# Optimization experiments

Measured on AMD Instinct MI355X. Metric: run time of the kernel, lower is better.

The kernel has to match this reference:

```python
import jax, jax.numpy as jnp
import numpy as np

B, S, E, H = 1, 2048, 4096, 32
D = E // H
MAX_POS = 2048
NEG_MASK = -66504.0
SCALE = float(np.sqrt(D))


def _rope(x, position_ids):
    # x: [B, S, H, D]; GPT-NeoX style rotate-half rotary embedding
    half = D // 2
    inv_freq = 1.0 / (10000.0 ** (jnp.arange(0, half, dtype=jnp.float32) * 2.0 / D))  # [D/2]
    ang = position_ids.astype(jnp.float32)[:, None] * inv_freq[None, :]               # [S, D/2]
    cos = jnp.cos(ang)[None, :, None, :]
    sin = jnp.sin(ang)[None, :, None, :]
    x1, x2 = x[..., :half], x[..., half:]
    return jnp.concatenate([x1 * cos - x2 * sin, x2 * cos + x1 * sin], axis=-1)


def setup_inputs() -> dict:
    key = jax.random.key(0)
    ks = jax.random.split(key, 9)
    s = 0.02
    return {
        "hidden_states": jax.random.normal(ks[0], (B, S, E), jnp.float32),
        "wq": jax.random.normal(ks[1], (E, E), jnp.float32) * s,
        "bq": jnp.zeros((E,), jnp.float32),
        "wk": jax.random.normal(ks[2], (E, E), jnp.float32) * s,
        "bk": jnp.zeros((E,), jnp.float32),
        "wv": jax.random.normal(ks[3], (E, E), jnp.float32) * s,
        "bv": jnp.zeros((E,), jnp.float32),
        "wo": jax.random.normal(ks[4], (E, E), jnp.float32) * s,
        "bo": jnp.zeros((E,), jnp.float32),
        "position_ids": jnp.arange(S, dtype=jnp.int32),
    }


def reference(hidden_states, wq, bq, wk, bk, wv, bv, wo, bo, position_ids):
    # QKV projections (nn.Linear: x @ W.T + b)
    q = hidden_states @ wq.T + bq
    k = hidden_states @ wk.T + bk
    v = hidden_states @ wv.T + bv
    # [B, S, H, D]
    q = q.reshape(B, S, H, D)
    k = k.reshape(B, S, H, D)
    v = v.reshape(B, S, H, D)
    # rotary embedding on key and query
    q = _rope(q, position_ids)
    k = _rope(k, position_ids)
    # [B, H, S, D]
    q = q.transpose(0, 2, 1, 3)
    k = k.transpose(0, 2, 1, 3)
    v = v.transpose(0, 2, 1, 3)
    # attention scores; causal mask added BEFORE dividing by scale (faithful to source)
    scores = jnp.einsum("bhqd,bhkd->bhqk", q, k)
    causal = (1.0 - jnp.tril(jnp.ones((S, S), jnp.float32))) * NEG_MASK  # [S, S]
    scores = (scores + causal[None, None]) / SCALE
    attn = jax.nn.softmax(scores.astype(jnp.float32), axis=-1).astype(q.dtype)
    ctx = jnp.einsum("bhqk,bhkd->bhqd", attn, v)
    ctx = ctx.transpose(0, 2, 1, 3).reshape(B, S, E)
    return ctx @ wo.T + bo
```

## Files before the change

### kernel.cpp

```cpp
#include <hip/hip_runtime.h>
#include <hip/hip_bf16.h>

constexpr int SEQ = 2048;
constexpr int EMB = 4096;
constexpr int NH  = 32;
constexpr int HD  = 128;
constexpr int HALF = 64;

typedef __bf16 bf16x8 __attribute__((ext_vector_type(8)));
typedef float  f32x4  __attribute__((ext_vector_type(4)));
using u16 = unsigned short;
typedef u16 ushort8 __attribute__((ext_vector_type(8)));
typedef u16 u16x4 __attribute__((ext_vector_type(4)));

__device__ inline float bf2f(u16 u) {
  union { unsigned int i; float f; } v; v.i = ((unsigned int)u) << 16; return v.f;
}
__device__ inline u16 f2bf(float f) {
  union { __bf16 b; u16 u; } v; v.b = (__bf16)f; return v.u;
}

#define GLL16(gp, lp) __builtin_amdgcn_global_load_lds( \
    (const __attribute__((address_space(1))) void*)(gp), \
    (__attribute__((address_space(3))) void*)(lp), 16, 0, 0)

__global__ void k_f32_to_bf16(const float* __restrict__ in, u16* __restrict__ out, int n) {
  int i = (blockIdx.x * blockDim.x + threadIdx.x) * 8;
  if (i >= n) return;
  f32x4 a = *(const f32x4*)(in + i);
  f32x4 b = *(const f32x4*)(in + i + 4);
  ushort8 o;
  o[0] = f2bf(a[0]); o[1] = f2bf(a[1]); o[2] = f2bf(a[2]); o[3] = f2bf(a[3]);
  o[4] = f2bf(b[0]); o[5] = f2bf(b[1]); o[6] = f2bf(b[2]); o[7] = f2bf(b[3]);
  *(ushort8*)(out + i) = o;
}

__global__ void k_rope_table(const int* __restrict__ pos, float* __restrict__ tab) {
  int idx = blockIdx.x * blockDim.x + threadIdx.x;
  if (idx >= SEQ * HALF) return;
  int s = idx >> 6, d = idx & 63;
  double invf = pow(10000.0, -(double)d / 64.0);
  double ang = (double)pos[s] * invf;
  tab[idx * 2]     = (float)cos(ang);
  tab[idx * 2 + 1] = (float)sin(ang);
}

__global__ void k_rope(u16* __restrict__ X, const float* __restrict__ tab, float scale) {
  int idx = blockIdx.x * blockDim.x + threadIdx.x;
  if (idx >= SEQ * NH * HALF) return;
  int d = idx & 63;
  int h = (idx >> 6) & 31;
  int s = idx >> 11;
  u16* p = X + (size_t)s * EMB + h * HD + d;
  float x1 = bf2f(p[0]), x2 = bf2f(p[HALF]);
  float c  = tab[(s * HALF + d) * 2];
  float sn = tab[(s * HALF + d) * 2 + 1];
  p[0]    = f2bf((x1 * c - x2 * sn) * scale);
  p[HALF] = f2bf((x2 * c + x1 * sn) * scale);
}

template<int TBM, int TBN>
__global__ __launch_bounds__(256) void k_gemm(
    const u16* __restrict__ A, const u16* __restrict__ W,
    const float* __restrict__ b0, const float* __restrict__ b1, const float* __restrict__ b2,
    void* __restrict__ C0, void* __restrict__ C1, void* __restrict__ C2,
    int M, int N, int K, int mode)
{
  constexpr int CH_A = TBM / 16, CH_B = TBN / 16;
  constexpr int CH_W = (CH_A + CH_B) / 4;
  constexpr int MA = TBM / 32, NB = TBN / 32;
  __shared__ alignas(16) u16 As[TBM * 32];
  __shared__ alignas(16) u16 Bs[TBN * 32];
  int tid = threadIdx.x;
  int lane = tid & 63, wid = tid >> 6;
  int wm = wid >> 1, wn = wid & 1;
  int l15 = lane & 15, lhi = lane >> 4;

  int nwg = gridDim.x * gridDim.y;
  int lin = blockIdx.y * gridDim.x + blockIdx.x;
  int cpx = nwg >> 3;
  int swz = (lin & 7) * cpx + (lin >> 3);
  int bx = swz % gridDim.x, by = swz / gridDim.x;
  int m0 = by * TBM, n0 = bx * TBN;

  f32x4 acc[MA][NB] = {};

  int srow = lane >> 2;
  int scol = (lane & 3) * 8;

  for (int k0 = 0; k0 < K; k0 += 32) {
    __syncthreads();
#pragma unroll
    for (int i = 0; i < CH_W; i++) {
      int chunk = wid * CH_W + i;
      if (chunk < CH_A) {
        int row = chunk * 16 + srow;
        GLL16(A + (size_t)(m0 + row) * K + k0 + scol, As + chunk * 512);
      } else {
        int c2 = chunk - CH_A;
        int row = c2 * 16 + srow;
        GLL16(W + (size_t)(n0 + row) * K + k0 + scol, Bs + c2 * 512);
      }
    }
    __syncthreads();

    bf16x8 af[MA], bfr[NB];
#pragma unroll
    for (int a = 0; a < MA; a++)
      af[a] = *(const bf16x8*)&As[(wm * (TBM / 2) + a * 16 + l15) * 32 + lhi * 8];
#pragma unroll
    for (int b = 0; b < NB; b++)
      bfr[b] = *(const bf16x8*)&Bs[(wn * (TBN / 2) + b * 16 + l15) * 32 + lhi * 8];
#pragma unroll
    for (int a = 0; a < MA; a++)
#pragma unroll
      for (int b = 0; b < NB; b++)
        acc[a][b] = __builtin_amdgcn_mfma_f32_16x16x32_bf16(af[a], bfr[b], acc[a][b], 0, 0, 0);
  }

  const float* bias = b0;
  void* Cout = C0;
  int mode_l = mode, Nn = N, n_base = n0;
  if (mode == 3) {
    int seg = n0 >> 12;
    Nn = EMB; n_base = n0 & 4095;
    if (seg == 0)      { bias = b0; Cout = C0; mode_l = 0; }
    else if (seg == 1) { bias = b1; Cout = C1; mode_l = 0; }
    else               { bias = b2; Cout = C2; mode_l = 2; }
  }

#pragma unroll
  for (int a = 0; a < MA; a++) {
    int m = m0 + wm * (TBM / 2) + a * 16 + lhi * 4;
#pragma unroll
    for (int b = 0; b < NB; b++) {
      int n = n_base + wn * (TBN / 2) + b * 16 + l15;
      float bs = bias[n];
      if (mode_l == 2) {
        u16x4 pk;
#pragma unroll
        for (int r = 0; r < 4; r++) pk[r] = f2bf(acc[a][b][r] + bs);
        *(u16x4*)&((u16*)Cout)[(size_t)n * M + m] = pk;
      } else if (mode_l == 1) {
#pragma unroll
        for (int r = 0; r < 4; r++)
          ((float*)Cout)[(size_t)(m + r) * Nn + n] = acc[a][b][r] + bs;
      } else {
#pragma unroll
        for (int r = 0; r < 4; r++)
          ((u16*)Cout)[(size_t)(m + r) * Nn + n] = f2bf(acc[a][b][r] + bs);
      }
    }
  }
}

constexpr int QB = 64, KVB = 64;

__global__ __launch_bounds__(256) void k_flash(
    const u16* __restrict__ Q, const u16* __restrict__ K, const u16* __restrict__ VT,
    u16* __restrict__ ctx)
{
  __shared__ alignas(16) u16 Ks[2][KVB * 128];
  __shared__ alignas(16) u16 Vt[2][HD * 64];
  __shared__ alignas(16) u16 Pl[4][16 * 64];

  int tid = threadIdx.x, lane = tid & 63, wid = tid >> 6;
  int l15 = lane & 15, lhi = lane >> 4;
  int h = blockIdx.y;

  auto stage = [&](int buf, int t2) {
    int kv = t2 * KVB;
#pragma unroll
    for (int it = 0; it < 4; it++) {
      int chunk = tid + it * 256;
      int r = chunk >> 4, bp = chunk & 15;
      GLL16(K + (size_t)(kv + r) * EMB + h * HD + (((bp - r) & 15) << 3), &Ks[buf][chunk * 8]);
    }
#pragma unroll
    for (int it = 0; it < 4; it++) {
      int chunk = tid + it * 256;
      int d = chunk >> 3, bp = chunk & 7;
      GLL16(VT + (size_t)(h * HD + d) * SEQ + kv + (((bp - d) & 7) << 3), &Vt[buf][chunk * 8]);
    }
  };

  for (int pi = 0; pi < 2; pi++) {
    int qb = pi ? (int)blockIdx.x : 31 - (int)blockIdx.x;
    int q0 = qb * QB;
    int qw = q0 + wid * 16;

    bf16x8 qf[4];
#pragma unroll
    for (int kc = 0; kc < 4; kc++)
      qf[kc] = *(const bf16x8*)&Q[(size_t)(qw + l15) * EMB + h * HD + kc * 32 + lhi * 8];

    f32x4 O[8] = {};
    float mrow[4], lrow[4];
#pragma unroll
    for (int r = 0; r < 4; r++) { mrow[r] = -3.0e38f; lrow[r] = 0.f; }

    int nt = qb + 1;
    __syncthreads();
    stage(0, 0);
    for (int t = 0; t < nt; t++) {
      __syncthreads();
      if (t + 1 < nt) stage((t + 1) & 1, t + 1);

      const u16* ks = Ks[t & 1];
      const u16* vt = Vt[t & 1];
      float p[4][4];
      bool need_mask = (t == nt - 1);
#pragma unroll
      for (int c = 0; c < 4; c++) {
        f32x4 s = {};
        int r0 = c * 16 + l15;
#pragma unroll
        for (int kc = 0; kc < 4; kc++) {
          bf16x8 kf = *(const bf16x8*)&ks[r0 * 128 + (((kc * 4 + lhi) + r0) & 15) * 8];
          s = __builtin_amdgcn_mfma_f32_16x16x32_bf16(qf[kc], kf, s, 0, 0, 0);
        }
#pragma unroll
        for (int r = 0; r < 4; r++) {
          float sv = s[r];
          if (need_mask) {
            int qg = qw + lhi * 4 + r;
            int kg = t * KVB + c * 16 + l15;
            if (kg > qg) sv = -3.0e38f;
          }
          p[c][r] = sv;
        }
      }
      float fscale[4];
#pragma unroll
      for (int r = 0; r < 4; r++) {
        float m = fmaxf(fmaxf(p[0][r], p[1][r]), fmaxf(p[2][r], p[3][r]));
#pragma unroll
        for (int x = 1; x < 16; x <<= 1) m = fmaxf(m, __shfl_xor(m, x, 64));
        float mnew = fmaxf(mrow[r], m);
        fscale[r] = __expf(mrow[r] - mnew);
        mrow[r] = mnew;
      }
#pragma unroll
      for (int c = 0; c < 4; c++)
#pragma unroll
        for (int r = 0; r < 4; r++)
          p[c][r] = __expf(p[c][r] - mrow[r]);
#pragma unroll
      for (int r = 0; r < 4; r++) {
        float s = p[0][r] + p[1][r] + p[2][r] + p[3][r];
#pragma unroll
        for (int x = 1; x < 16; x <<= 1) s += __shfl_xor(s, x, 64);
        lrow[r] = lrow[r] * fscale[r] + s;
      }
#pragma unroll
      for (int d = 0; d < 8; d++)
#pragma unroll
        for (int r = 0; r < 4; r++)
          O[d][r] *= fscale[r];
#pragma unroll
      for (int c = 0; c < 4; c++) {
        int kb = c * 2 + (l15 >> 3), klo = l15 & 7;
#pragma unroll
        for (int r = 0; r < 4; r++) {
          int q = lhi * 4 + r;
          Pl[wid][q * 64 + ((kb + (q >> 1)) & 7) * 8 + klo] = f2bf(p[c][r]);
        }
      }
#pragma unroll
      for (int ks2 = 0; ks2 < 2; ks2++) {
        int kb = ks2 * 4 + lhi;
        bf16x8 pf = *(const bf16x8*)&Pl[wid][l15 * 64 + ((kb + (l15 >> 1)) & 7) * 8];
#pragma unroll
        for (int ds = 0; ds < 8; ds++) {
          int d = ds * 16 + l15;
          bf16x8 vf = *(const bf16x8*)&vt[d * 64 + ((kb + d) & 7) * 8];
          O[ds] = __builtin_amdgcn_mfma_f32_16x16x32_bf16(pf, vf, O[ds], 0, 0, 0);
        }
      }
    }

#pragma unroll
    for (int r = 0; r < 4; r++) {
      float inv = 1.f / lrow[r];
      int qg = q0 + wid * 16 + lhi * 4 + r;
#pragma unroll
      for (int ds = 0; ds < 8; ds++)
        ctx[(size_t)qg * EMB + h * HD + ds * 16 + l15] = f2bf(O[ds][r] * inv);
    }
  }
}

extern "C" void kernel_launch(void* const* d_in, const int* in_sizes, int n_in,
                              void* d_out, int out_size, void* d_ws, size_t ws_size,
                              hipStream_t stream) {
  const float* hs = (const float*)d_in[0];
  const float* wq = (const float*)d_in[1];
  const float* bq = (const float*)d_in[2];
  const float* wk = (const float*)d_in[3];
  const float* bk = (const float*)d_in[4];
  const float* wv = (const float*)d_in[5];
  const float* bv = (const float*)d_in[6];
  const float* wo = (const float*)d_in[7];
  const float* bo = (const float*)d_in[8];
  const int*  pos = (const int*)d_in[9];

  const size_t SE = (size_t)SEQ * EMB;
  const size_t EE = (size_t)EMB * EMB;
  const float qscale = 1.0f / 11.313708498984761f;

  char* ws = (char*)d_ws;
  size_t off = 0;
  auto alloc = [&](size_t b) { size_t o = off; off += (b + 255) & ~(size_t)255; return o; };

  size_t need_fused = ((SE * 2 + 255) & ~255ULL) + ((EE * 6 + 255) & ~255ULL) +
                      3 * ((SE * 2 + 255) & ~255ULL) + ((size_t)SEQ * HALF * 8 + 255);
  bool fused = ws_size >= need_fused + 4096;

  u16*  hsb = (u16*)(ws + alloc(SE * 2));
  u16*  wb  = (u16*)(ws + alloc(fused ? EE * 6 : EE * 2));
  u16*  Qb  = (u16*)(ws + alloc(SE * 2));
  u16*  Kb  = (u16*)(ws + alloc(SE * 2));
  u16*  VTb = (u16*)(ws + alloc(SE * 2));
  float* tab = (float*)(ws + alloc((size_t)SEQ * HALF * 2 * 4));
  u16*  ctxb = hsb;

  dim3 cb(256);
  k_f32_to_bf16<<<dim3(SE / 2048), cb, 0, stream>>>(hs, hsb, (int)SE);
  k_rope_table<<<dim3(SEQ * HALF / 256), cb, 0, stream>>>(pos, tab);

  if (fused) {
    k_f32_to_bf16<<<dim3(EE / 2048), cb, 0, stream>>>(wq, wb, (int)EE);
    k_f32_to_bf16<<<dim3(EE / 2048), cb, 0, stream>>>(wk, wb + EE, (int)EE);
    k_f32_to_bf16<<<dim3(EE / 2048), cb, 0, stream>>>(wv, wb + 2 * EE, (int)EE);
    k_gemm<128, 128><<<dim3(96, 16), cb, 0, stream>>>(
        hsb, wb, bq, bk, bv, (void*)Qb, (void*)Kb, (void*)VTb, SEQ, 3 * EMB, EMB, 3);
  } else {
    k_f32_to_bf16<<<dim3(EE / 2048), cb, 0, stream>>>(wq, wb, (int)EE);
    k_gemm<128, 128><<<dim3(32, 16), cb, 0, stream>>>(
        hsb, wb, bq, bq, bq, (void*)Qb, nullptr, nullptr, SEQ, EMB, EMB, 0);
    k_f32_to_bf16<<<dim3(EE / 2048), cb, 0, stream>>>(wk, wb, (int)EE);
    k_gemm<128, 128><<<dim3(32, 16), cb, 0, stream>>>(
        hsb, wb, bk, bk, bk, (void*)Kb, nullptr, nullptr, SEQ, EMB, EMB, 0);
    k_f32_to_bf16<<<dim3(EE / 2048), cb, 0, stream>>>(wv, wb, (int)EE);
    k_gemm<128, 128><<<dim3(32, 16), cb, 0, stream>>>(
        hsb, wb, bv, bv, bv, (void*)VTb, nullptr, nullptr, SEQ, EMB, EMB, 2);
  }

  k_rope<<<dim3(SEQ * NH * HALF / 256), cb, 0, stream>>>(Qb, tab, qscale);
  k_rope<<<dim3(SEQ * NH * HALF / 256), cb, 0, stream>>>(Kb, tab, 1.0f);

  k_flash<<<dim3(16, NH), cb, 0, stream>>>(Qb, Kb, VTb, ctxb);

  k_f32_to_bf16<<<dim3(EE / 2048), cb, 0, stream>>>(wo, wb, (int)EE);
  k_gemm<64, 128><<<dim3(32, 32), cb, 0, stream>>>(
      ctxb, wb, bo, bo, bo, d_out, nullptr, nullptr, SEQ, EMB, EMB, 1);
}
```

Baseline: 577.4 us.

## Double-buffer GEMM LDS tiles, enlarge QKV tiles, and remap blocks per XCD

The GEMM kernel now double-buffers its A/B LDS tiles, so the global-to-LDS load for the next K step is issued before the MFMAs on the current one, with one barrier per iteration. The warp layout is templated: the QKV projection uses 128x256 tiles with 8 waves (512 threads), and the output projection keeps 64x128 with 4 waves. Block-to-tile mapping moves to a 1D grid that gives each XCD a contiguous range of N columns to improve L2 reuse. The larger tile and doubled LDS raise register and LDS pressure, which may lower occupancy. The mapping also assumes the N tile count divides by 8.

```diff
diff --git a/kernel.cpp b/kernel.cpp
--- a/kernel.cpp
+++ b/kernel.cpp
@@ -59,28 +59,28 @@
   p[HALF] = f2bf((x2 * c + x1 * sn) * scale);
 }
 
-template<int TBM, int TBN>
-__global__ __launch_bounds__(256) void k_gemm(
+template<int TBM, int TBN, int WM, int WN>
+__global__ __launch_bounds__(WM * WN * 64) void k_gemm(
     const u16* __restrict__ A, const u16* __restrict__ W,
     const float* __restrict__ b0, const float* __restrict__ b1, const float* __restrict__ b2,
     void* __restrict__ C0, void* __restrict__ C1, void* __restrict__ C2,
     int M, int N, int K, int mode)
 {
   constexpr int CH_A = TBM / 16, CH_B = TBN / 16;
-  constexpr int CH_W = (CH_A + CH_B) / 4;
-  constexpr int MA = TBM / 32, NB = TBN / 32;
-  __shared__ alignas(16) u16 As[TBM * 32];
-  __shared__ alignas(16) u16 Bs[TBN * 32];
+  constexpr int CH_W = (CH_A + CH_B) / (WM * WN);
+  constexpr int MA = TBM / WM / 16, NB = TBN / WN / 16;
+  __shared__ alignas(16) u16 As[2][TBM * 32];
+  __shared__ alignas(16) u16 Bs[2][TBN * 32];
   int tid = threadIdx.x;
   int lane = tid & 63, wid = tid >> 6;
-  int wm = wid >> 1, wn = wid & 1;
+  int wm = wid / WN, wn = wid % WN;
   int l15 = lane & 15, lhi = lane >> 4;
 
-  int nwg = gridDim.x * gridDim.y;
-  int lin = blockIdx.y * gridDim.x + blockIdx.x;
-  int cpx = nwg >> 3;
-  int swz = (lin & 7) * cpx + (lin >> 3);
-  int bx = swz % gridDim.x, by = swz / gridDim.x;
+  int NBY = M / TBM, NBX = N / TBN;
+  int wg = blockIdx.x;
+  int xcd = wg & 7, s = wg >> 3;
+  int by = s % NBY, bxl = s / NBY;
+  int bx = xcd * (NBX >> 3) + bxl;
   int m0 = by * TBM, n0 = bx * TBN;
 
   f32x4 acc[MA][NB] = {};
@@ -88,29 +88,36 @@
   int srow = lane >> 2;
   int scol = (lane & 3) * 8;
 
-  for (int k0 = 0; k0 < K; k0 += 32) {
-    __syncthreads();
+  auto stage = [&](int buf, int k0) {
 #pragma unroll
     for (int i = 0; i < CH_W; i++) {
       int chunk = wid * CH_W + i;
       if (chunk < CH_A) {
         int row = chunk * 16 + srow;
-        GLL16(A + (size_t)(m0 + row) * K + k0 + scol, As + chunk * 512);
+        GLL16(A + (size_t)(m0 + row) * K + k0 + scol, &As[buf][chunk * 512]);
       } else {
         int c2 = chunk - CH_A;
         int row = c2 * 16 + srow;
-        GLL16(W + (size_t)(n0 + row) * K + k0 + scol, Bs + c2 * 512);
-      }
-    }
+        GLL16(W + (size_t)(n0 + row) * K + k0 + scol, &Bs[buf][c2 * 512]);
+      }
+    }
+  };
+
+  int KT = K / 32;
+  stage(0, 0);
+  for (int t = 0; t < KT; t++) {
     __syncthreads();
-
+    if (t + 1 < KT) stage((t + 1) & 1, (t + 1) * 32);
+
+    const u16* as = As[t & 1];
+    const u16* bs = Bs[t & 1];
     bf16x8 af[MA], bfr[NB];
 #pragma unroll
     for (int a = 0; a < MA; a++)
-      af[a] = *(const bf16x8*)&As[(wm * (TBM / 2) + a * 16 + l15) * 32 + lhi * 8];
+      af[a] = *(const bf16x8*)&as[(wm * (TBM / WM) + a * 16 + l15) * 32 + lhi * 8];
 #pragma unroll
     for (int b = 0; b < NB; b++)
-      bfr[b] = *(const bf16x8*)&Bs[(wn * (TBN / 2) + b * 16 + l15) * 32 + lhi * 8];
+      bfr[b] = *(const bf16x8*)&bs[(wn * (TBN / WN) + b * 16 + l15) * 32 + lhi * 8];
 #pragma unroll
     for (int a = 0; a < MA; a++)
 #pragma unroll
@@ -131,24 +138,24 @@
 
 #pragma unroll
   for (int a = 0; a < MA; a++) {
-    int m = m0 + wm * (TBM / 2) + a * 16 + lhi * 4;
+    int m = m0 + wm * (TBM / WM) + a * 16 + lhi * 4;
 #pragma unroll
     for (int b = 0; b < NB; b++) {
-      int n = n_base + wn * (TBN / 2) + b * 16 + l15;
-      float bs = bias[n];
+      int n = n_base + wn * (TBN / WN) + b * 16 + l15;
+      float bs2 = bias[n];
       if (mode_l == 2) {
         u16x4 pk;
 #pragma unroll
-        for (int r = 0; r < 4; r++) pk[r] = f2bf(acc[a][b][r] + bs);
+        for (int r = 0; r < 4; r++) pk[r] = f2bf(acc[a][b][r] + bs2);
         *(u16x4*)&((u16*)Cout)[(size_t)n * M + m] = pk;
       } else if (mode_l == 1) {
 #pragma unroll
         for (int r = 0; r < 4; r++)
-          ((float*)Cout)[(size_t)(m + r) * Nn + n] = acc[a][b][r] + bs;
+          ((float*)Cout)[(size_t)(m + r) * Nn + n] = acc[a][b][r] + bs2;
       } else {
 #pragma unroll
         for (int r = 0; r < 4; r++)
-          ((u16*)Cout)[(size_t)(m + r) * Nn + n] = f2bf(acc[a][b][r] + bs);
+          ((u16*)Cout)[(size_t)(m + r) * Nn + n] = f2bf(acc[a][b][r] + bs2);
       }
     }
   }
@@ -332,17 +339,17 @@
     k_f32_to_bf16<<<dim3(EE / 2048), cb, 0, stream>>>(wq, wb, (int)EE);
     k_f32_to_bf16<<<dim3(EE / 2048), cb, 0, stream>>>(wk, wb + EE, (int)EE);
     k_f32_to_bf16<<<dim3(EE / 2048), cb, 0, stream>>>(wv, wb + 2 * EE, (int)EE);
-    k_gemm<128, 128><<<dim3(96, 16), cb, 0, stream>>>(
+    k_gemm<128, 256, 2, 4><<<dim3(768), dim3(512), 0, stream>>>(
         hsb, wb, bq, bk, bv, (void*)Qb, (void*)Kb, (void*)VTb, SEQ, 3 * EMB, EMB, 3);
   } else {
     k_f32_to_bf16<<<dim3(EE / 2048), cb, 0, stream>>>(wq, wb, (int)EE);
-    k_gemm<128, 128><<<dim3(32, 16), cb, 0, stream>>>(
+    k_gemm<128, 256, 2, 4><<<dim3(256), dim3(512), 0, stream>>>(
         hsb, wb, bq, bq, bq, (void*)Qb, nullptr, nullptr, SEQ, EMB, EMB, 0);
     k_f32_to_bf16<<<dim3(EE / 2048), cb, 0, stream>>>(wk, wb, (int)EE);
-    k_gemm<128, 128><<<dim3(32, 16), cb, 0, stream>>>(
+    k_gemm<128, 256, 2, 4><<<dim3(256), dim3(512), 0, stream>>>(
         hsb, wb, bk, bk, bk, (void*)Kb, nullptr, nullptr, SEQ, EMB, EMB, 0);
     k_f32_to_bf16<<<dim3(EE / 2048), cb, 0, stream>>>(wv, wb, (int)EE);
-    k_gemm<128, 128><<<dim3(32, 16), cb, 0, stream>>>(
+    k_gemm<128, 256, 2, 4><<<dim3(256), dim3(512), 0, stream>>>(
         hsb, wb, bv, bv, bv, (void*)VTb, nullptr, nullptr, SEQ, EMB, EMB, 2);
   }
 
@@ -352,6 +359,6 @@
   k_flash<<<dim3(16, NH), cb, 0, stream>>>(Qb, Kb, VTb, ctxb);
 
   k_f32_to_bf16<<<dim3(EE / 2048), cb, 0, stream>>>(wo, wb, (int)EE);
-  k_gemm<64, 128><<<dim3(32, 32), cb, 0, stream>>>(
+  k_gemm<64, 128, 2, 2><<<dim3(1024), cb, 0, stream>>>(
       ctxb, wb, bo, bo, bo, d_out, nullptr, nullptr, SEQ, EMB, EMB, 1);
 }
```

Result: faster. 553.5 us (-4.1%).
